# Optimization experiments

Hardware: AMD Instinct MI355X
Metric: run time of the kernel (lower is better)

The kernel has to match this reference:

```python
import jax, jax.numpy as jnp
import numpy as np

DIM = 96
NUM_HEADS = 3
WINDOW = (2, 7, 7)


def _relative_position_index(ws):
    # same construction as the torch buffer, done once in numpy (static)
    wd, wh, ww = ws
    coords = np.stack(np.meshgrid(np.arange(wd), np.arange(wh), np.arange(ww), indexing='ij'))
    coords_flat = coords.reshape(3, -1)                      # [3, N]
    rel = coords_flat[:, :, None] - coords_flat[:, None, :]  # [3, N, N]
    rel = rel.transpose(1, 2, 0).astype(np.int64)            # [N, N, 3]
    rel[:, :, 0] += wd - 1
    rel[:, :, 1] += wh - 1
    rel[:, :, 2] += ww - 1
    rel[:, :, 0] *= (2 * wh - 1) * (2 * ww - 1)
    rel[:, :, 1] *= 2 * ww - 1
    return rel.sum(-1)                                       # [N, N]


def setup_inputs() -> dict:
    key = jax.random.key(0)
    ks = jax.random.split(key, 6)
    B_ = 4096
    N = WINDOW[0] * WINDOW[1] * WINDOW[2]  # 98
    C = DIM
    table_len = (2 * WINDOW[0] - 1) * (2 * WINDOW[1] - 1) * (2 * WINDOW[2] - 1)  # 507
    x = jax.random.normal(ks[0], (B_, N, C), dtype=jnp.float32)
    qkv_w = jax.random.normal(ks[1], (3 * C, C), dtype=jnp.float32) * (1.0 / np.sqrt(C))
    qkv_b = jnp.zeros((3 * C,), dtype=jnp.float32)
    proj_w = jax.random.normal(ks[2], (C, C), dtype=jnp.float32) * (1.0 / np.sqrt(C))
    proj_b = jnp.zeros((C,), dtype=jnp.float32)
    bias_table = jax.random.normal(ks[3], (table_len, NUM_HEADS), dtype=jnp.float32) * 0.02
    rel_index = jnp.asarray(_relative_position_index(WINDOW), dtype=jnp.int32)  # [N, N]
    return {"x": x, "qkv_w": qkv_w, "qkv_b": qkv_b, "proj_w": proj_w,
            "proj_b": proj_b, "bias_table": bias_table, "rel_index": rel_index}


def reference(x, qkv_w, qkv_b, proj_w, proj_b, bias_table, rel_index):
    B_, N, C = x.shape
    H = NUM_HEADS
    hd = C // H
    scale = hd ** (-0.5)
    qkv = x @ qkv_w.T + qkv_b                        # [B_, N, 3C]
    qkv = qkv.reshape(B_, N, 3, H, hd).transpose(2, 0, 3, 1, 4)  # [3, B_, H, N, hd]
    q, k, v = qkv[0], qkv[1], qkv[2]
    attn = jnp.einsum('bhnd,bhmd->bhnm', q, k) * scale           # [B_, H, N, N]
    bias = bias_table[rel_index.reshape(-1)].reshape(N, N, H).transpose(2, 0, 1)  # [H, N, N]
    attn = jax.nn.softmax(attn + bias[None], axis=-1)
    out = jnp.einsum('bhnm,bhmd->bhnd', attn, v)                 # [B_, H, N, hd]
    out = out.transpose(0, 2, 1, 3).reshape(B_, N, C)
    return out @ proj_w.T + proj_b
```

## Files before the change

kernel.cpp:

```cpp
#include <hip/hip_runtime.h>
#include <stdint.h>

#define NTOK 98
#define CDIM 96
#define LDK 104
#define LDV 120

typedef __bf16 bf16x8 __attribute__((ext_vector_type(8)));
typedef __bf16 bf16x2 __attribute__((ext_vector_type(2)));
typedef float f32x4 __attribute__((ext_vector_type(4)));

__device__ __forceinline__ uint16_t f2bfbits(float f) {
  uint32_t u = __builtin_bit_cast(uint32_t, f);
  u += 0x7FFFu + ((u >> 16) & 1u);
  return (uint16_t)(u >> 16);
}

__device__ __forceinline__ uint32_t pk2(float a, float b) {
  bf16x2 t;
  t[0] = (__bf16)a;
  t[1] = (__bf16)b;
  return __builtin_bit_cast(uint32_t, t);
}

__device__ __forceinline__ bf16x8 cvt8(const float* p) {
  float4 a = *(const float4*)p;
  float4 b = *(const float4*)(p + 4);
  bf16x8 r;
  r[0] = (__bf16)a.x; r[1] = (__bf16)a.y; r[2] = (__bf16)a.z; r[3] = (__bf16)a.w;
  r[4] = (__bf16)b.x; r[5] = (__bf16)b.y; r[6] = (__bf16)b.z; r[7] = (__bf16)b.w;
  return r;
}

__device__ __forceinline__ bf16x8 rechunk(uint32_t e0, uint32_t e1, uint32_t o0,
                                          uint32_t o1, int selA, int selB,
                                          bool lowq) {
  int a0 = __builtin_amdgcn_ds_bpermute(selA, (int)e0);
  int a1 = __builtin_amdgcn_ds_bpermute(selA, (int)e1);
  int b0 = __builtin_amdgcn_ds_bpermute(selB, (int)e0);
  int b1 = __builtin_amdgcn_ds_bpermute(selB, (int)e1);
  int a0o = __builtin_amdgcn_ds_bpermute(selA, (int)o0);
  int a1o = __builtin_amdgcn_ds_bpermute(selA, (int)o1);
  int b0o = __builtin_amdgcn_ds_bpermute(selB, (int)o0);
  int b1o = __builtin_amdgcn_ds_bpermute(selB, (int)o1);
  uint4 w;
  w.x = (uint32_t)(lowq ? a0 : a0o);
  w.y = (uint32_t)(lowq ? a1 : a1o);
  w.z = (uint32_t)(lowq ? b0 : b0o);
  w.w = (uint32_t)(lowq ? b1 : b1o);
  return __builtin_bit_cast(bf16x8, w);
}

__global__ void precompute(const float* __restrict__ qkv_w,
                           const float* __restrict__ proj_w,
                           const float* __restrict__ bias_table,
                           const int* __restrict__ rel_index,
                           uint16_t* __restrict__ qkv_wp,
                           uint16_t* __restrict__ proj_wp,
                           float* __restrict__ bias_full) {
  int t = blockIdx.x * blockDim.x + threadIdx.x;
  int stride = gridDim.x * blockDim.x;
  for (int f = t; f < 18 * 3 * 4 * 16 * 8; f += stride) {
    int j = f & 7, l16 = (f >> 3) & 15, quad = (f >> 7) & 3, ktnt = f >> 9;
    int kt = ktnt % 3, nt = ktnt / 3;
    qkv_wp[f] = f2bfbits(qkv_w[(nt * 16 + l16) * CDIM + kt * 32 + quad * 8 + j]);
  }
  for (int f = t; f < 6 * 3 * 4 * 16 * 8; f += stride) {
    int j = f & 7, l16 = (f >> 3) & 15, quad = (f >> 7) & 3, ktnt = f >> 9;
    int kt = ktnt % 3, nt = ktnt / 3;
    proj_wp[f] = f2bfbits(proj_w[(nt * 16 + l16) * CDIM + kt * 32 + quad * 8 + j]);
  }
  for (int f = t; f < 3 * 128 * 112; f += stride) {
    int col = f % 112;
    int hr = f / 112;
    int row = hr & 127;
    int h = hr >> 7;
    float v = 0.f;
    if (row < NTOK && col < NTOK)
      v = bias_table[rel_index[row * NTOK + col] * 3 + h];
    bias_full[f] = v;
  }
}

__global__ __launch_bounds__(256, 3) void wattn3d(
    const float* __restrict__ x, const float* __restrict__ qkv_b,
    const float* __restrict__ proj_b, const uint16_t* __restrict__ qkv_wp,
    const uint16_t* __restrict__ proj_wp, const float* __restrict__ bias_full,
    float* __restrict__ out) {
  __shared__ __align__(16) char smem[43552];
  __bf16* k_lds = (__bf16*)smem;
  __bf16* vT = (__bf16*)(smem + 20384);

  const int tid = threadIdx.x;
  const int wave = tid >> 6;
  const int lane = tid & 63;
  const int quad = lane >> 4;
  const int l16 = lane & 15;
  const int b = blockIdx.x;
  const int rowbase = wave * 32;
  const float scale = 0.17677669529663687f;

  const int selA = (l16 | (((2 * quad) & 3) << 4)) << 2;
  const int selB = (l16 | (((2 * quad + 1) & 3) << 4)) << 2;
  const bool lowq = quad < 2;

  for (int i = tid; i < CDIM * 8; i += 256) {
    int d = i >> 3, tk = 112 + (i & 7);
    vT[d * LDV + tk] = (__bf16)0.0f;
  }
  if (tid < 32) ((uint32_t*)(smem + 43424))[tid] = 0u;

  const float* xb = x + (size_t)b * NTOK * CDIM;

  bf16x8 a_x[2][3];
#pragma unroll
  for (int mt = 0; mt < 2; ++mt) {
    int row = rowbase + mt * 16 + l16;
#pragma unroll
    for (int kt = 0; kt < 3; ++kt) {
      if (row < NTOK) {
        a_x[mt][kt] = cvt8(xb + row * CDIM + kt * 32 + quad * 8);
      } else {
        bf16x8 z;
#pragma unroll
        for (int j = 0; j < 8; ++j) z[j] = (__bf16)0.0f;
        a_x[mt][kt] = z;
      }
    }
  }

  uint32_t qpk[2][6][2];
#pragma unroll
  for (int nt = 0; nt < 6; ++nt) {
    bf16x8 bw[3];
#pragma unroll
    for (int kt = 0; kt < 3; ++kt)
      bw[kt] = *(const bf16x8*)(qkv_wp + (((nt * 3 + kt) * 4 + quad) * 16 + l16) * 8);
    float4 qb4 = *(const float4*)&qkv_b[nt * 16 + quad * 4];
#pragma unroll
    for (int mt = 0; mt < 2; ++mt) {
      f32x4 acc = {0.f, 0.f, 0.f, 0.f};
#pragma unroll
      for (int kt = 0; kt < 3; ++kt)
        acc = __builtin_amdgcn_mfma_f32_16x16x32_bf16(bw[kt], a_x[mt][kt], acc, 0, 0, 0);
      qpk[mt][nt][0] = pk2((acc[0] + qb4.x) * scale, (acc[1] + qb4.y) * scale);
      qpk[mt][nt][1] = pk2((acc[2] + qb4.z) * scale, (acc[3] + qb4.w) * scale);
    }
  }

#pragma unroll
  for (int nt = 6; nt < 18; ++nt) {
    bf16x8 bw[3];
#pragma unroll
    for (int kt = 0; kt < 3; ++kt)
      bw[kt] = *(const bf16x8*)(qkv_wp + (((nt * 3 + kt) * 4 + quad) * 16 + l16) * 8);
    float bn = qkv_b[nt * 16 + l16];
#pragma unroll
    for (int mt = 0; mt < 2; ++mt) {
      f32x4 acc = {0.f, 0.f, 0.f, 0.f};
#pragma unroll
      for (int kt = 0; kt < 3; ++kt)
        acc = __builtin_amdgcn_mfma_f32_16x16x32_bf16(a_x[mt][kt], bw[kt], acc, 0, 0, 0);
      if (nt < 12) {
        int colb = (nt - 6) * 16 + l16;
#pragma unroll
        for (int i = 0; i < 4; ++i) {
          int row = rowbase + mt * 16 + quad * 4 + i;
          if (row < NTOK) k_lds[row * LDK + colb] = (__bf16)(acc[i] + bn);
        }
      } else {
        int d = (nt - 12) * 16 + l16;
        int t0 = rowbase + mt * 16 + quad * 4;
        if (t0 < 112) {
          uint2 pk;
          pk.x = pk2(acc[0] + bn, acc[1] + bn);
          pk.y = pk2(acc[2] + bn, acc[3] + bn);
          *(uint2*)&vT[d * LDV + t0] = pk;
        }
      }
    }
  }
  __syncthreads();

  uint32_t opk[2][3][4];
  float rs[2];

#pragma unroll
  for (int h = 0; h < 3; ++h) {
    bf16x8 qf[2];
#pragma unroll
    for (int mt = 0; mt < 2; ++mt)
      qf[mt] = rechunk(qpk[mt][2 * h][0], qpk[mt][2 * h][1],
                       qpk[mt][2 * h + 1][0], qpk[mt][2 * h + 1][1],
                       selA, selB, lowq);

    f32x4 sacc[2][7];
#pragma unroll
    for (int nt = 0; nt < 7; ++nt) {
      bf16x8 ak = *(bf16x8*)&k_lds[(nt * 16 + l16) * LDK + h * 32 + quad * 8];
#pragma unroll
      for (int mt = 0; mt < 2; ++mt) {
        f32x4 z = {0.f, 0.f, 0.f, 0.f};
        sacc[mt][nt] = __builtin_amdgcn_mfma_f32_16x16x32_bf16(ak, qf[mt], z, 0, 0, 0);
      }
    }

#pragma unroll
    for (int mt = 0; mt < 2; ++mt) {
      const int qrow = rowbase + mt * 16 + l16;
      const float* brow = bias_full + ((size_t)h * 128 + qrow) * 112 + quad * 4;
      float mx = -1e30f;
#pragma unroll
      for (int nt = 0; nt < 7; ++nt) {
        float4 b4 = *(const float4*)(brow + nt * 16);
        float bv[4] = {b4.x, b4.y, b4.z, b4.w};
#pragma unroll
        for (int i = 0; i < 4; ++i) {
          float s = sacc[mt][nt][i] + bv[i];
          if (nt == 6 && !(quad == 0 && i < 2)) s = -1e30f;
          sacc[mt][nt][i] = s;
          mx = fmaxf(mx, s);
        }
      }
      mx = fmaxf(mx, __shfl_xor(mx, 16));
      mx = fmaxf(mx, __shfl_xor(mx, 32));
      float sum = 0.f;
#pragma unroll
      for (int nt = 0; nt < 7; ++nt)
#pragma unroll
        for (int i = 0; i < 4; ++i) {
          float p = __expf(sacc[mt][nt][i] - mx);
          sacc[mt][nt][i] = p;
          sum += p;
        }
      sum += __shfl_xor(sum, 16);
      sum += __shfl_xor(sum, 32);
      rs[mt] = 1.f / sum;
    }

    f32x4 oacc[2][2];
#pragma unroll
    for (int mt = 0; mt < 2; ++mt)
#pragma unroll
      for (int nh = 0; nh < 2; ++nh) {
        f32x4 z = {0.f, 0.f, 0.f, 0.f};
        oacc[mt][nh] = z;
      }
#pragma unroll
    for (int kt2 = 0; kt2 < 4; ++kt2) {
      bf16x8 av[2];
#pragma unroll
      for (int nh = 0; nh < 2; ++nh)
        av[nh] = *(bf16x8*)&vT[(h * 32 + nh * 16 + l16) * LDV + kt2 * 32 + quad * 8];
#pragma unroll
      for (int mt = 0; mt < 2; ++mt) {
        uint32_t e0 = pk2(sacc[mt][2 * kt2][0], sacc[mt][2 * kt2][1]);
        uint32_t e1 = pk2(sacc[mt][2 * kt2][2], sacc[mt][2 * kt2][3]);
        uint32_t o0 = 0u, o1 = 0u;
        if (kt2 < 3) {
          o0 = pk2(sacc[mt][2 * kt2 + 1][0], sacc[mt][2 * kt2 + 1][1]);
          o1 = pk2(sacc[mt][2 * kt2 + 1][2], sacc[mt][2 * kt2 + 1][3]);
        }
        bf16x8 pf = rechunk(e0, e1, o0, o1, selA, selB, lowq);
#pragma unroll
        for (int nh = 0; nh < 2; ++nh)
          oacc[mt][nh] = __builtin_amdgcn_mfma_f32_16x16x32_bf16(av[nh], pf, oacc[mt][nh], 0, 0, 0);
      }
    }

#pragma unroll
    for (int mt = 0; mt < 2; ++mt) {
      float r = rs[mt];
      opk[mt][h][0] = pk2(oacc[mt][0][0] * r, oacc[mt][0][1] * r);
      opk[mt][h][1] = pk2(oacc[mt][0][2] * r, oacc[mt][0][3] * r);
      opk[mt][h][2] = pk2(oacc[mt][1][0] * r, oacc[mt][1][1] * r);
      opk[mt][h][3] = pk2(oacc[mt][1][2] * r, oacc[mt][1][3] * r);
    }
  }

  float* outb = out + (size_t)b * NTOK * CDIM;
#pragma unroll
  for (int mt = 0; mt < 2; ++mt) {
    bf16x8 of[3];
#pragma unroll
    for (int kt = 0; kt < 3; ++kt)
      of[kt] = rechunk(opk[mt][kt][0], opk[mt][kt][1], opk[mt][kt][2],
                       opk[mt][kt][3], selA, selB, lowq);
    const int qrow = rowbase + mt * 16 + l16;
#pragma unroll
    for (int nt = 0; nt < 6; ++nt) {
      f32x4 acc = {0.f, 0.f, 0.f, 0.f};
#pragma unroll
      for (int kt = 0; kt < 3; ++kt) {
        bf16x8 aw = *(const bf16x8*)(proj_wp + (((nt * 3 + kt) * 4 + quad) * 16 + l16) * 8);
        acc = __builtin_amdgcn_mfma_f32_16x16x32_bf16(aw, of[kt], acc, 0, 0, 0);
      }
      if (qrow < NTOK) {
        float4 pb4 = *(const float4*)&proj_b[nt * 16 + quad * 4];
        float4 o4;
        o4.x = acc[0] + pb4.x;
        o4.y = acc[1] + pb4.y;
        o4.z = acc[2] + pb4.z;
        o4.w = acc[3] + pb4.w;
        *(float4*)&outb[(size_t)qrow * CDIM + nt * 16 + quad * 4] = o4;
      }
    }
  }
}

extern "C" void kernel_launch(void* const* d_in, const int* in_sizes, int n_in,
                              void* d_out, int out_size, void* d_ws, size_t ws_size,
                              hipStream_t stream) {
  (void)n_in; (void)out_size; (void)ws_size;
  const float* x = (const float*)d_in[0];
  const float* qkv_w = (const float*)d_in[1];
  const float* qkv_b = (const float*)d_in[2];
  const float* proj_w = (const float*)d_in[3];
  const float* proj_b = (const float*)d_in[4];
  const float* bias_table = (const float*)d_in[5];
  const int* rel_index = (const int*)d_in[6];
  float* out = (float*)d_out;

  uint16_t* qkv_wp = (uint16_t*)d_ws;
  uint16_t* proj_wp = (uint16_t*)((char*)d_ws + 55296);
  float* bias_full = (float*)((char*)d_ws + 73728);

  precompute<<<dim3(64), dim3(256), 0, stream>>>(qkv_w, proj_w, bias_table,
                                                 rel_index, qkv_wp, proj_wp,
                                                 bias_full);
  int Bwin = in_sizes[0] / (NTOK * CDIM);
  wattn3d<<<dim3(Bwin), dim3(256), 0, stream>>>(x, qkv_b, proj_b, qkv_wp,
                                                proj_wp, bias_full, out);
}
```

Baseline: 390.5 us.

## Use 16x16x16 bf16 MFMA to drop cross-lane rechunk shuffles and shrink LDS

Replaces the 16x16x32 MFMAs in QK^T, PV and the output projection with 16x16x16 bf16 MFMAs. The accumulator layout then feeds straight into the next MFMA operand, so all ds_bpermute rechunk shuffles go away. K is now stored row-contiguous with packed writes, LDS padding shrinks, and occupancy is raised to 4 blocks per SIMD. Softmax moves to exp2 by folding log2(e) into the scale and the bias table, and the proj weights are repacked for the K=16 layout. The cost is twice as many smaller MFMA issues and tighter register limits from the higher occupancy.

```diff
diff --git a/kernel.cpp b/kernel.cpp
--- a/kernel.cpp
+++ b/kernel.cpp
@@ -3,12 +3,19 @@
 
 #define NTOK 98
 #define CDIM 96
-#define LDK 104
-#define LDV 120
+#define LDK 100
+#define LDV 108
 
 typedef __bf16 bf16x8 __attribute__((ext_vector_type(8)));
 typedef __bf16 bf16x2 __attribute__((ext_vector_type(2)));
 typedef float f32x4 __attribute__((ext_vector_type(4)));
+typedef short s16x4 __attribute__((ext_vector_type(4)));
+
+#if __has_builtin(__builtin_amdgcn_exp2f)
+#define EXP2F(x) __builtin_amdgcn_exp2f(x)
+#else
+#define EXP2F(x) __expf((x)*0.6931471805599453f)
+#endif
 
 __device__ __forceinline__ uint16_t f2bfbits(float f) {
   uint32_t u = __builtin_bit_cast(uint32_t, f);
@@ -21,6 +28,12 @@
   t[0] = (__bf16)a;
   t[1] = (__bf16)b;
   return __builtin_bit_cast(uint32_t, t);
+}
+__device__ __forceinline__ s16x4 pks4(float a, float b, float c, float d) {
+  uint2 u;
+  u.x = pk2(a, b);
+  u.y = pk2(c, d);
+  return __builtin_bit_cast(s16x4, u);
 }
 
 __device__ __forceinline__ bf16x8 cvt8(const float* p) {
@@ -32,23 +45,14 @@
   return r;
 }
 
-__device__ __forceinline__ bf16x8 rechunk(uint32_t e0, uint32_t e1, uint32_t o0,
-                                          uint32_t o1, int selA, int selB,
-                                          bool lowq) {
-  int a0 = __builtin_amdgcn_ds_bpermute(selA, (int)e0);
-  int a1 = __builtin_amdgcn_ds_bpermute(selA, (int)e1);
-  int b0 = __builtin_amdgcn_ds_bpermute(selB, (int)e0);
-  int b1 = __builtin_amdgcn_ds_bpermute(selB, (int)e1);
-  int a0o = __builtin_amdgcn_ds_bpermute(selA, (int)o0);
-  int a1o = __builtin_amdgcn_ds_bpermute(selA, (int)o1);
-  int b0o = __builtin_amdgcn_ds_bpermute(selB, (int)o0);
-  int b1o = __builtin_amdgcn_ds_bpermute(selB, (int)o1);
-  uint4 w;
-  w.x = (uint32_t)(lowq ? a0 : a0o);
-  w.y = (uint32_t)(lowq ? a1 : a1o);
-  w.z = (uint32_t)(lowq ? b0 : b0o);
-  w.w = (uint32_t)(lowq ? b1 : b1o);
-  return __builtin_bit_cast(bf16x8, w);
+__device__ __forceinline__ f32x4 mfma16(s16x4 a, s16x4 b, f32x4 c) {
+#if __has_builtin(__builtin_amdgcn_mfma_f32_16x16x16bf16_1k)
+  return __builtin_amdgcn_mfma_f32_16x16x16bf16_1k(a, b, c, 0, 0, 0);
+#else
+  f32x4 d;
+  asm("v_mfma_f32_16x16x16_bf16 %0, %1, %2, %3" : "=v"(d) : "v"(a), "v"(b), "v"(c));
+  return d;
+#endif
 }
 
 __global__ void precompute(const float* __restrict__ qkv_w,
@@ -65,10 +69,10 @@
     int kt = ktnt % 3, nt = ktnt / 3;
     qkv_wp[f] = f2bfbits(qkv_w[(nt * 16 + l16) * CDIM + kt * 32 + quad * 8 + j]);
   }
-  for (int f = t; f < 6 * 3 * 4 * 16 * 8; f += stride) {
-    int j = f & 7, l16 = (f >> 3) & 15, quad = (f >> 7) & 3, ktnt = f >> 9;
-    int kt = ktnt % 3, nt = ktnt / 3;
-    proj_wp[f] = f2bfbits(proj_w[(nt * 16 + l16) * CDIM + kt * 32 + quad * 8 + j]);
+  for (int f = t; f < 6 * 6 * 4 * 16 * 4; f += stride) {
+    int j = f & 3, l16 = (f >> 2) & 15, quad = (f >> 6) & 3, kgnt = f >> 8;
+    int kg = kgnt % 6, nt = kgnt / 6;
+    proj_wp[f] = f2bfbits(proj_w[(nt * 16 + l16) * CDIM + kg * 16 + quad * 4 + j]);
   }
   for (int f = t; f < 3 * 128 * 112; f += stride) {
     int col = f % 112;
@@ -77,19 +81,19 @@
     int h = hr >> 7;
     float v = 0.f;
     if (row < NTOK && col < NTOK)
-      v = bias_table[rel_index[row * NTOK + col] * 3 + h];
+      v = bias_table[rel_index[row * NTOK + col] * 3 + h] * 1.4426950408889634f;
     bias_full[f] = v;
   }
 }
 
-__global__ __launch_bounds__(256, 3) void wattn3d(
+__global__ __launch_bounds__(256, 4) void wattn3d(
     const float* __restrict__ x, const float* __restrict__ qkv_b,
     const float* __restrict__ proj_b, const uint16_t* __restrict__ qkv_wp,
     const uint16_t* __restrict__ proj_wp, const float* __restrict__ bias_full,
     float* __restrict__ out) {
-  __shared__ __align__(16) char smem[43552];
+  __shared__ __align__(16) char smem[40352];
   __bf16* k_lds = (__bf16*)smem;
-  __bf16* vT = (__bf16*)(smem + 20384);
+  __bf16* vT = (__bf16*)(smem + 19600);
 
   const int tid = threadIdx.x;
   const int wave = tid >> 6;
@@ -98,17 +102,9 @@
   const int l16 = lane & 15;
   const int b = blockIdx.x;
   const int rowbase = wave * 32;
-  const float scale = 0.17677669529663687f;
-
-  const int selA = (l16 | (((2 * quad) & 3) << 4)) << 2;
-  const int selB = (l16 | (((2 * quad + 1) & 3) << 4)) << 2;
-  const bool lowq = quad < 2;
-
-  for (int i = tid; i < CDIM * 8; i += 256) {
-    int d = i >> 3, tk = 112 + (i & 7);
-    vT[d * LDV + tk] = (__bf16)0.0f;
-  }
-  if (tid < 32) ((uint32_t*)(smem + 43424))[tid] = 0u;
+  const float scale = 0.17677669529663687f * 1.4426950408889634f;
+
+  if (tid < 4) ((uint32_t*)(smem + 40336))[tid] = 0u;
 
   const float* xb = x + (size_t)b * NTOK * CDIM;
 
@@ -129,27 +125,36 @@
     }
   }
 
-  uint32_t qpk[2][6][2];
-#pragma unroll
-  for (int nt = 0; nt < 6; ++nt) {
+  s16x4 qf[2][6];
+#pragma unroll
+  for (int nt = 0; nt < 12; ++nt) {
     bf16x8 bw[3];
 #pragma unroll
     for (int kt = 0; kt < 3; ++kt)
       bw[kt] = *(const bf16x8*)(qkv_wp + (((nt * 3 + kt) * 4 + quad) * 16 + l16) * 8);
-    float4 qb4 = *(const float4*)&qkv_b[nt * 16 + quad * 4];
+    float4 b4 = *(const float4*)&qkv_b[nt * 16 + quad * 4];
 #pragma unroll
     for (int mt = 0; mt < 2; ++mt) {
       f32x4 acc = {0.f, 0.f, 0.f, 0.f};
 #pragma unroll
       for (int kt = 0; kt < 3; ++kt)
         acc = __builtin_amdgcn_mfma_f32_16x16x32_bf16(bw[kt], a_x[mt][kt], acc, 0, 0, 0);
-      qpk[mt][nt][0] = pk2((acc[0] + qb4.x) * scale, (acc[1] + qb4.y) * scale);
-      qpk[mt][nt][1] = pk2((acc[2] + qb4.z) * scale, (acc[3] + qb4.w) * scale);
-    }
-  }
-
-#pragma unroll
-  for (int nt = 6; nt < 18; ++nt) {
+      if (nt < 6) {
+        qf[mt][nt] = pks4((acc[0] + b4.x) * scale, (acc[1] + b4.y) * scale,
+                          (acc[2] + b4.z) * scale, (acc[3] + b4.w) * scale);
+      } else {
+        int tok = rowbase + mt * 16 + l16;
+        if (tok < NTOK) {
+          uint2 pk;
+          pk.x = pk2(acc[0] + b4.x, acc[1] + b4.y);
+          pk.y = pk2(acc[2] + b4.z, acc[3] + b4.w);
+          *(uint2*)&k_lds[tok * LDK + (nt - 6) * 16 + quad * 4] = pk;
+        }
+      }
+    }
+  }
+#pragma unroll
+  for (int nt = 12; nt < 18; ++nt) {
     bf16x8 bw[3];
 #pragma unroll
     for (int kt = 0; kt < 3; ++kt)
@@ -161,50 +166,35 @@
 #pragma unroll
       for (int kt = 0; kt < 3; ++kt)
         acc = __builtin_amdgcn_mfma_f32_16x16x32_bf16(a_x[mt][kt], bw[kt], acc, 0, 0, 0);
-      if (nt < 12) {
-        int colb = (nt - 6) * 16 + l16;
-#pragma unroll
-        for (int i = 0; i < 4; ++i) {
-          int row = rowbase + mt * 16 + quad * 4 + i;
-          if (row < NTOK) k_lds[row * LDK + colb] = (__bf16)(acc[i] + bn);
-        }
-      } else {
-        int d = (nt - 12) * 16 + l16;
-        int t0 = rowbase + mt * 16 + quad * 4;
-        if (t0 < 112) {
-          uint2 pk;
-          pk.x = pk2(acc[0] + bn, acc[1] + bn);
-          pk.y = pk2(acc[2] + bn, acc[3] + bn);
-          *(uint2*)&vT[d * LDV + t0] = pk;
-        }
+      int t0 = rowbase + mt * 16 + quad * 4;
+      if (t0 < LDV) {
+        uint2 pk;
+        pk.x = pk2(acc[0] + bn, acc[1] + bn);
+        pk.y = pk2(acc[2] + bn, acc[3] + bn);
+        *(uint2*)&vT[((nt - 12) * 16 + l16) * LDV + t0] = pk;
       }
     }
   }
   __syncthreads();
 
-  uint32_t opk[2][3][4];
-  float rs[2];
-
+  s16x4 og[2][6];
 #pragma unroll
   for (int h = 0; h < 3; ++h) {
-    bf16x8 qf[2];
-#pragma unroll
-    for (int mt = 0; mt < 2; ++mt)
-      qf[mt] = rechunk(qpk[mt][2 * h][0], qpk[mt][2 * h][1],
-                       qpk[mt][2 * h + 1][0], qpk[mt][2 * h + 1][1],
-                       selA, selB, lowq);
-
     f32x4 sacc[2][7];
 #pragma unroll
     for (int nt = 0; nt < 7; ++nt) {
-      bf16x8 ak = *(bf16x8*)&k_lds[(nt * 16 + l16) * LDK + h * 32 + quad * 8];
+      const __bf16* krow = &k_lds[(nt * 16 + l16) * LDK + h * 32 + quad * 4];
+      s16x4 ak0 = *(const s16x4*)krow;
+      s16x4 ak1 = *(const s16x4*)(krow + 16);
 #pragma unroll
       for (int mt = 0; mt < 2; ++mt) {
         f32x4 z = {0.f, 0.f, 0.f, 0.f};
-        sacc[mt][nt] = __builtin_amdgcn_mfma_f32_16x16x32_bf16(ak, qf[mt], z, 0, 0, 0);
-      }
-    }
-
+        f32x4 s0 = mfma16(ak0, qf[mt][2 * h], z);
+        sacc[mt][nt] = mfma16(ak1, qf[mt][2 * h + 1], s0);
+      }
+    }
+
+    float rs[2];
 #pragma unroll
     for (int mt = 0; mt < 2; ++mt) {
       const int qrow = rowbase + mt * 16 + l16;
@@ -229,7 +219,7 @@
       for (int nt = 0; nt < 7; ++nt)
 #pragma unroll
         for (int i = 0; i < 4; ++i) {
-          float p = __expf(sacc[mt][nt][i] - mx);
+          float p = EXP2F(sacc[mt][nt][i] - mx);
           sacc[mt][nt][i] = p;
           sum += p;
         }
@@ -247,53 +237,41 @@
         oacc[mt][nh] = z;
       }
 #pragma unroll
-    for (int kt2 = 0; kt2 < 4; ++kt2) {
-      bf16x8 av[2];
-#pragma unroll
-      for (int nh = 0; nh < 2; ++nh)
-        av[nh] = *(bf16x8*)&vT[(h * 32 + nh * 16 + l16) * LDV + kt2 * 32 + quad * 8];
-#pragma unroll
-      for (int mt = 0; mt < 2; ++mt) {
-        uint32_t e0 = pk2(sacc[mt][2 * kt2][0], sacc[mt][2 * kt2][1]);
-        uint32_t e1 = pk2(sacc[mt][2 * kt2][2], sacc[mt][2 * kt2][3]);
-        uint32_t o0 = 0u, o1 = 0u;
-        if (kt2 < 3) {
-          o0 = pk2(sacc[mt][2 * kt2 + 1][0], sacc[mt][2 * kt2 + 1][1]);
-          o1 = pk2(sacc[mt][2 * kt2 + 1][2], sacc[mt][2 * kt2 + 1][3]);
-        }
-        bf16x8 pf = rechunk(e0, e1, o0, o1, selA, selB, lowq);
-#pragma unroll
-        for (int nh = 0; nh < 2; ++nh)
-          oacc[mt][nh] = __builtin_amdgcn_mfma_f32_16x16x32_bf16(av[nh], pf, oacc[mt][nh], 0, 0, 0);
+    for (int g = 0; g < 7; ++g) {
+      s16x4 pf[2];
+#pragma unroll
+      for (int mt = 0; mt < 2; ++mt)
+        pf[mt] = pks4(sacc[mt][g][0], sacc[mt][g][1], sacc[mt][g][2], sacc[mt][g][3]);
+#pragma unroll
+      for (int nh = 0; nh < 2; ++nh) {
+        s16x4 av = *(const s16x4*)&vT[(h * 32 + nh * 16 + l16) * LDV + g * 16 + quad * 4];
+#pragma unroll
+        for (int mt = 0; mt < 2; ++mt)
+          oacc[mt][nh] = mfma16(av, pf[mt], oacc[mt][nh]);
       }
     }
 
 #pragma unroll
     for (int mt = 0; mt < 2; ++mt) {
       float r = rs[mt];
-      opk[mt][h][0] = pk2(oacc[mt][0][0] * r, oacc[mt][0][1] * r);
-      opk[mt][h][1] = pk2(oacc[mt][0][2] * r, oacc[mt][0][3] * r);
-      opk[mt][h][2] = pk2(oacc[mt][1][0] * r, oacc[mt][1][1] * r);
-      opk[mt][h][3] = pk2(oacc[mt][1][2] * r, oacc[mt][1][3] * r);
+      og[mt][2 * h + 0] = pks4(oacc[mt][0][0] * r, oacc[mt][0][1] * r,
+                               oacc[mt][0][2] * r, oacc[mt][0][3] * r);
+      og[mt][2 * h + 1] = pks4(oacc[mt][1][0] * r, oacc[mt][1][1] * r,
+                               oacc[mt][1][2] * r, oacc[mt][1][3] * r);
     }
   }
 
   float* outb = out + (size_t)b * NTOK * CDIM;
 #pragma unroll
   for (int mt = 0; mt < 2; ++mt) {
-    bf16x8 of[3];
-#pragma unroll
-    for (int kt = 0; kt < 3; ++kt)
-      of[kt] = rechunk(opk[mt][kt][0], opk[mt][kt][1], opk[mt][kt][2],
-                       opk[mt][kt][3], selA, selB, lowq);
     const int qrow = rowbase + mt * 16 + l16;
 #pragma unroll
     for (int nt = 0; nt < 6; ++nt) {
       f32x4 acc = {0.f, 0.f, 0.f, 0.f};
 #pragma unroll
-      for (int kt = 0; kt < 3; ++kt) {
-        bf16x8 aw = *(const bf16x8*)(proj_wp + (((nt * 3 + kt) * 4 + quad) * 16 + l16) * 8);
-        acc = __builtin_amdgcn_mfma_f32_16x16x32_bf16(aw, of[kt], acc, 0, 0, 0);
+      for (int kg = 0; kg < 6; ++kg) {
+        s16x4 aw = *(const s16x4*)(proj_wp + (((nt * 6 + kg) * 4 + quad) * 16 + l16) * 4);
+        acc = mfma16(aw, og[mt][kg], acc);
       }
       if (qrow < NTOK) {
         float4 pb4 = *(const float4*)&proj_b[nt * 16 + quad * 4];
```

New measurement: 396.8 us. No clear change (+1.6%).
